# Kernel tuning notes

Hardware: AMD Instinct MI355X
Metric: run time of the kernel (lower is better)

## Reference

```python
import jax, jax.numpy as jnp
import numpy as np

DIM = 1024
NUM_HEADS = 16
HEAD_DIM = DIM // NUM_HEADS
SCALE = 1.0 / float(np.sqrt(HEAD_DIM))


def setup_inputs() -> dict:
    key = jax.random.key(0)
    ks = jax.random.split(key, 8)
    b, n = 1, 4096
    x = jax.random.normal(ks[0], (b, n, DIM), dtype=jnp.float32)
    cos = jax.random.uniform(ks[1], (b, n, HEAD_DIM // 2), dtype=jnp.float32)
    sin = jax.random.uniform(ks[2], (b, n, HEAD_DIM // 2), dtype=jnp.float32)
    # qkv Linear(dim, 3*dim) and proj Linear(dim, dim); store weights as [in, out]
    w_qkv = jax.random.normal(ks[3], (DIM, 3 * DIM), dtype=jnp.float32) * (1.0 / np.sqrt(DIM))
    b_qkv = jax.random.normal(ks[4], (3 * DIM,), dtype=jnp.float32) * 0.01
    w_proj = jax.random.normal(ks[5], (DIM, DIM), dtype=jnp.float32) * (1.0 / np.sqrt(DIM))
    b_proj = jax.random.normal(ks[6], (DIM,), dtype=jnp.float32) * 0.01
    return {"x": x, "cos": cos, "sin": sin, "w_qkv": w_qkv, "b_qkv": b_qkv,
            "w_proj": w_proj, "b_proj": b_proj}


def _rotate_half(t):
    t1, t2 = jnp.split(t, 2, axis=-1)
    return jnp.concatenate([-t2, t1], axis=-1)


def reference(x, cos, sin, w_qkv, b_qkv, w_proj, b_proj):
    b, n, d = x.shape
    qkv = x @ w_qkv + b_qkv                      # [b, n, 3d]
    q, k, v = jnp.split(qkv, 3, axis=-1)
    # [b, n, h, hd] layout (avoids explicit transposes; einsum handles head axis)
    q = q.reshape(b, n, NUM_HEADS, HEAD_DIM)
    k = k.reshape(b, n, NUM_HEADS, HEAD_DIM)
    v = v.reshape(b, n, NUM_HEADS, HEAD_DIM)
    # RoPE: cos/sin [b, n, hd/2] -> [b, n, 1, hd], broadcast over heads
    cos_f = jnp.concatenate([cos, cos], axis=-1)[:, :, None, :]
    sin_f = jnp.concatenate([sin, sin], axis=-1)[:, :, None, :]
    q = q * cos_f + _rotate_half(q) * sin_f
    k = k * cos_f + _rotate_half(k) * sin_f
    # SDPA (non-causal, no dropout in eval)
    scores = jnp.einsum("bqhd,bkhd->bhqk", q, k) * SCALE
    attn = jax.nn.softmax(scores, axis=-1)
    out = jnp.einsum("bhqk,bkhd->bqhd", attn, v).reshape(b, n, d)
    return out @ w_proj + b_proj
```

## Files before the change

### kernel.cpp

```cpp
#include <hip/hip_runtime.h>
#include <hip/hip_bf16.h>
#include <cstdint>


#define TOK 4096
#define DIM_ 1024
#define NHEAD 16
#define HDIM 64
#define N3 3072
#define SCALE_LOG2E 0.18033688011112042f

typedef __bf16 bf16_t;
typedef bf16_t bf16x8 __attribute__((ext_vector_type(8)));
typedef float floatx4 __attribute__((ext_vector_type(4)));

__device__ __forceinline__ void async_ld16(const bf16_t* g, bf16_t* l) {
  __builtin_amdgcn_global_load_lds(
      (const __attribute__((address_space(1))) void*)(g),
      (__attribute__((address_space(3))) void*)(l), 16, 0, 0);
}

__device__ __forceinline__ uint32_t pk2(float lo, float hi) {
  union { bf16_t b[2]; uint32_t u; } p;
  p.b[0] = (bf16_t)lo; p.b[1] = (bf16_t)hi;
  return p.u;
}

__global__ __launch_bounds__(256) void k_prep(
    const float* __restrict__ x, const float* __restrict__ w_qkv,
    const float* __restrict__ w_proj, bf16_t* __restrict__ xb,
    bf16_t* __restrict__ wqkvT, bf16_t* __restrict__ wprojT) {
  __shared__ float tile[32][33];
  const int b = blockIdx.x;
  if (b < 4096) {
    int i = b * 256 + threadIdx.x;
    float4 v = ((const float4*)x)[i];
    union { bf16_t bb[4]; uint64_t u; } p;
    p.bb[0] = (bf16_t)v.x; p.bb[1] = (bf16_t)v.y;
    p.bb[2] = (bf16_t)v.z; p.bb[3] = (bf16_t)v.w;
    ((uint64_t*)xb)[i] = p.u;
    return;
  }
  const float* in; bf16_t* out; int R, C, c0, r0;
  if (b < 7168) {
    int bb = b - 4096; in = w_qkv; out = wqkvT; R = 1024; C = 3072;
    c0 = (bb % 96) * 32; r0 = (bb / 96) * 32;
  } else {
    int bb = b - 7168; in = w_proj; out = wprojT; R = 1024; C = 1024;
    c0 = (bb % 32) * 32; r0 = (bb / 32) * 32;
  }
  int tx = threadIdx.x & 31, ty = threadIdx.x >> 5;
#pragma unroll
  for (int i = 0; i < 4; i++) {
    int r = ty + i * 8;
    tile[r][tx] = in[(size_t)(r0 + r) * C + c0 + tx];
  }
  __syncthreads();
#pragma unroll
  for (int i = 0; i < 4; i++) {
    int c = ty + i * 8;
    out[(size_t)(c0 + c) * R + r0 + tx] = (bf16_t)tile[tx][c];
  }
}

__global__ __launch_bounds__(256) void k_qkv(
    const bf16_t* __restrict__ A,
    const bf16_t* __restrict__ Bt,
    const float* __restrict__ bias,
    const float* __restrict__ cs,
    const float* __restrict__ sn,
    bf16_t* __restrict__ qb, bf16_t* __restrict__ kb, bf16_t* __restrict__ vT) {
  constexpr int K = 1024, BK = 32;
  __shared__ bf16_t As[128 * BK] __attribute__((aligned(16)));
  __shared__ bf16_t Bs[128 * BK] __attribute__((aligned(16)));
  const int t = threadIdx.x;
  const int lane = t & 63, w = t >> 6;
  const int lrow = lane & 15, quad = lane >> 4;
  const int m0 = blockIdx.y * 128, n0 = blockIdx.x * 128;
  const int wm = (w >> 1) * 64, wn = (w & 1) * 64;

  const floatx4 ZV = {0.f, 0.f, 0.f, 0.f};
  floatx4 acc[4][4];
#pragma unroll
  for (int i = 0; i < 4; i++)
#pragma unroll
    for (int j = 0; j < 4; j++) acc[i][j] = ZV;

  for (int kt = 0; kt < K; kt += BK) {
#pragma unroll
    for (int r = 0; r < 2; r++) {
      int idx = r * 256 + t;
      int lbase = (r * 256 + w * 64) * 8;
      async_ld16(&A[(size_t)(m0 + (idx >> 2)) * K + kt + (idx & 3) * 8], &As[lbase]);
      async_ld16(&Bt[(size_t)(n0 + (idx >> 2)) * K + kt + (idx & 3) * 8], &Bs[lbase]);
    }
    __syncthreads();
    bf16x8 af[4], bf[4];
#pragma unroll
    for (int i = 0; i < 4; i++)
      af[i] = *(const bf16x8*)&As[(wm + i * 16 + lrow) * BK + quad * 8];
#pragma unroll
    for (int i = 0; i < 4; i++)
      bf[i] = *(const bf16x8*)&Bs[(wn + i * 16 + lrow) * BK + quad * 8];
#pragma unroll
    for (int mi = 0; mi < 4; mi++)
#pragma unroll
      for (int ni = 0; ni < 4; ni++)
        acc[mi][ni] = __builtin_amdgcn_mfma_f32_16x16x32_bf16(af[mi], bf[ni], acc[mi][ni], 0, 0, 0);
    __syncthreads();
  }

  const int c0 = n0 + wn;
  const int seg = c0 >> 10;
  const int h = (c0 & 1023) >> 6;
  float bv[4];
#pragma unroll
  for (int ni = 0; ni < 4; ni++) bv[ni] = bias[c0 + ni * 16 + lrow];

  if (seg < 2) {
    bf16_t* base = ((seg == 0) ? qb : kb) + (size_t)h * TOK * HDIM;
    const float qs = (seg == 0) ? SCALE_LOG2E : 1.0f;
#pragma unroll
    for (int mi = 0; mi < 4; mi++) {
#pragma unroll
      for (int reg = 0; reg < 4; reg++) {
        const int r = m0 + wm + mi * 16 + quad * 4 + reg;
        const float c_lo = cs[r * 32 + lrow];
        const float c_hi = cs[r * 32 + 16 + lrow];
        const float s_lo = sn[r * 32 + lrow];
        const float s_hi = sn[r * 32 + 16 + lrow];
        const float v0 = acc[mi][0][reg] + bv[0];
        const float v1 = acc[mi][1][reg] + bv[1];
        const float v2 = acc[mi][2][reg] + bv[2];
        const float v3 = acc[mi][3][reg] + bv[3];
        const float o0 = (v0 * c_lo - v2 * s_lo) * qs;
        const float o1 = (v1 * c_hi - v3 * s_hi) * qs;
        const float o2 = (v2 * c_lo + v0 * s_lo) * qs;
        const float o3 = (v3 * c_hi + v1 * s_hi) * qs;
        bf16_t* rp = base + (size_t)r * HDIM + lrow;
        rp[0]  = (bf16_t)o0;
        rp[16] = (bf16_t)o1;
        rp[32] = (bf16_t)o2;
        rp[48] = (bf16_t)o3;
      }
    }
  } else {
    bf16_t* base = vT + (size_t)h * HDIM * TOK;
#pragma unroll
    for (int mi = 0; mi < 4; mi++) {
      const int rbase = m0 + wm + mi * 16 + quad * 4;
#pragma unroll
      for (int ni = 0; ni < 4; ni++) {
        union { bf16_t b[4]; uint64_t u; } p;
#pragma unroll
        for (int reg = 0; reg < 4; reg++) p.b[reg] = (bf16_t)(acc[mi][ni][reg] + bv[ni]);
        *(uint64_t*)&base[(size_t)(ni * 16 + lrow) * TOK + rbase] = p.u;
      }
    }
  }
}

__global__ __launch_bounds__(256, 2) void k_attn(
    const bf16_t* __restrict__ qb, const bf16_t* __restrict__ kb,
    const bf16_t* __restrict__ vT, bf16_t* __restrict__ ao) {
  __shared__ bf16_t Ks[2][64 * 64] __attribute__((aligned(16)));
  __shared__ bf16_t Vs[3][64 * 64] __attribute__((aligned(16)));
  __shared__ float Lmrg[128];
  const int t = threadIdx.x, lane = t & 63, w = t >> 6;
  const int lrow = lane & 15, quad = lane >> 4;
  const int qg = w & 1, kh = w >> 1;
  const int h = blockIdx.x & 15;
  const int q0 = (blockIdx.x >> 4) * 128;
  const bf16_t* qh = qb + (size_t)h * TOK * HDIM;
  const bf16_t* khp = kb + (size_t)h * TOK * HDIM;
  const bf16_t* vhp = vT + (size_t)h * HDIM * TOK;

  const int ksrc = (t >> 3) * HDIM + (((t & 7) ^ ((t >> 3) & 7)) * 8);
  const int vsrc = (t >> 3) * TOK + (((t & 7) ^ ((t >> 3) & 7)) * 8);

  bf16x8 qf[4][2];
#pragma unroll
  for (int ni = 0; ni < 4; ni++)
#pragma unroll
    for (int ks = 0; ks < 2; ks++)
      qf[ni][ks] = *(const bf16x8*)&qh[(size_t)(q0 + qg * 64 + ni * 16 + lrow) * HDIM + ks * 32 + quad * 8];

  const floatx4 ZV = {0.f, 0.f, 0.f, 0.f};
  floatx4 o[4][4];
  floatx4 lacc[4] = {ZV, ZV, ZV, ZV};
#pragma unroll
  for (int d = 0; d < 4; d++)
#pragma unroll
    for (int ni = 0; ni < 4; ni++) o[d][ni] = ZV;

#pragma unroll
  for (int r = 0; r < 2; r++) {
    async_ld16(&khp[(size_t)(r * 32) * HDIM + ksrc], &Ks[0][r * 2048 + t * 8]);
    async_ld16(&vhp[(size_t)(r * 32) * TOK + vsrc], &Vs[0][r * 2048 + t * 8]);
  }

  bf16x8 pf[4];
  bf16x8 vf[4];

  for (int it = 0; it < TOK / 64; ++it) {
    const int b = it & 1;
    __syncthreads();
    if (it + 1 < TOK / 64) {
      const int j1 = (it + 1) * 64;
      const int vs1 = (it + 1) % 3;
#pragma unroll
      for (int r = 0; r < 2; r++) {
        async_ld16(&khp[((size_t)j1 + r * 32) * HDIM + ksrc], &Ks[b ^ 1][r * 2048 + t * 8]);
        async_ld16(&vhp[(size_t)(r * 32) * TOK + j1 + vsrc], &Vs[vs1][r * 2048 + t * 8]);
      }
    }

    if (it > 0) {
#pragma unroll
      for (int dt = 0; dt < 4; dt++)
#pragma unroll
        for (int ni = 0; ni < 4; ni++)
          o[dt][ni] = __builtin_amdgcn_mfma_f32_16x16x32_bf16(vf[dt], pf[ni], o[dt][ni], 0, 0, 0);
    }

    floatx4 s[2][4];
#pragma unroll
    for (int mi = 0; mi < 2; mi++)
#pragma unroll
      for (int ni = 0; ni < 4; ni++) s[mi][ni] = ZV;
#pragma unroll
    for (int ks = 0; ks < 2; ks++)
#pragma unroll
      for (int mi = 0; mi < 2; mi++) {
        bf16x8 kf = *(const bf16x8*)&Ks[b][(kh * 32 + mi * 16 + lrow) * 64 + (((ks * 4 + quad) ^ (lrow & 7)) * 8)];
#pragma unroll
        for (int ni = 0; ni < 4; ni++)
          s[mi][ni] = __builtin_amdgcn_mfma_f32_16x16x32_bf16(kf, qf[ni][ks], s[mi][ni], 0, 0, 0);
      }

#pragma unroll
    for (int dt = 0; dt < 4; dt++)
      vf[dt] = *(const bf16x8*)&Vs[it % 3][(dt * 16 + lrow) * 64 + (((kh * 4 + quad) ^ (lrow & 7)) * 8)];

#pragma unroll
    for (int mi = 0; mi < 2; mi++)
#pragma unroll
      for (int ni = 0; ni < 4; ni++) {
#pragma unroll
        for (int reg = 0; reg < 4; reg++)
          s[mi][ni][reg] = __builtin_amdgcn_exp2f(s[mi][ni][reg]);
        lacc[ni] += s[mi][ni];
      }

#pragma unroll
    for (int ni = 0; ni < 4; ni++) {
      uint32_t A0 = pk2(s[0][ni][0], s[0][ni][1]);
      uint32_t A1 = pk2(s[0][ni][2], s[0][ni][3]);
      uint32_t B0 = pk2(s[1][ni][0], s[1][ni][1]);
      uint32_t B1 = pk2(s[1][ni][2], s[1][ni][3]);
      auto u0 = __builtin_amdgcn_permlane32_swap(A0, B0, false, false);
      auto u1 = __builtin_amdgcn_permlane32_swap(A1, B1, false, false);
      auto c0 = __builtin_amdgcn_permlane16_swap(u0[0], u0[1], false, false);
      auto c1 = __builtin_amdgcn_permlane16_swap(u1[0], u1[1], false, false);
      union { uint32_t d[4]; bf16x8 v; } pp;
      pp.d[0] = c0[0]; pp.d[1] = c1[0]; pp.d[2] = c0[1]; pp.d[3] = c1[1];
      pf[ni] = pp.v;
    }
  }

#pragma unroll
  for (int dt = 0; dt < 4; dt++)
#pragma unroll
    for (int ni = 0; ni < 4; ni++)
      o[dt][ni] = __builtin_amdgcn_mfma_f32_16x16x32_bf16(vf[dt], pf[ni], o[dt][ni], 0, 0, 0);

  __syncthreads();
  float* Mrg = (qg == 0) ? (float*)&Ks[0][0] : (float*)&Vs[0][0];
  float lq[4];
#pragma unroll
  for (int ni = 0; ni < 4; ni++) {
    float l = lacc[ni][0] + lacc[ni][1] + lacc[ni][2] + lacc[ni][3];
    l += __shfl_xor(l, 16, 64);
    l += __shfl_xor(l, 32, 64);
    lq[ni] = l;
  }
  if (kh == 1) {
#pragma unroll
    for (int ni = 0; ni < 4; ni++) {
#pragma unroll
      for (int dt = 0; dt < 4; dt++)
        *(floatx4*)&Mrg[(ni * 16 + lrow) * 64 + dt * 16 + quad * 4] = o[dt][ni];
      if (quad == 0) Lmrg[qg * 64 + ni * 16 + lrow] = lq[ni];
    }
  }
  __syncthreads();
  if (kh == 0) {
#pragma unroll
    for (int ni = 0; ni < 4; ni++) {
      const float l = lq[ni] + Lmrg[qg * 64 + ni * 16 + lrow];
      const float inv = 1.0f / l;
      const int qrow = q0 + qg * 64 + ni * 16 + lrow;
#pragma unroll
      for (int dt = 0; dt < 4; dt++) {
        floatx4 ov = *(const floatx4*)&Mrg[(ni * 16 + lrow) * 64 + dt * 16 + quad * 4];
        union { bf16_t b4[4]; uint64_t u; } p;
#pragma unroll
        for (int reg = 0; reg < 4; reg++) p.b4[reg] = (bf16_t)((o[dt][ni][reg] + ov[reg]) * inv);
        *(uint64_t*)&ao[(size_t)qrow * DIM_ + h * HDIM + dt * 16 + quad * 4] = p.u;
      }
    }
  }
}

__global__ __launch_bounds__(256) void k_proj(
    const bf16_t* __restrict__ A,
    const bf16_t* __restrict__ Bt,
    const float* __restrict__ bias, float* __restrict__ out) {
  constexpr int K = 1024, BK = 32;
  __shared__ bf16_t As[64 * BK] __attribute__((aligned(16)));
  __shared__ bf16_t Bs[128 * BK] __attribute__((aligned(16)));
  const int t = threadIdx.x;
  const int lane = t & 63, w = t >> 6;
  const int lrow = lane & 15, quad = lane >> 4;
  const int m0 = blockIdx.y * 64, n0 = blockIdx.x * 128;
  const int wm = (w >> 1) * 32, wn = (w & 1) * 64;

  const floatx4 ZV = {0.f, 0.f, 0.f, 0.f};
  floatx4 acc[2][4];
#pragma unroll
  for (int i = 0; i < 2; i++)
#pragma unroll
    for (int j = 0; j < 4; j++) acc[i][j] = ZV;

  for (int kt = 0; kt < K; kt += BK) {
    async_ld16(&A[(size_t)(m0 + (t >> 2)) * K + kt + (t & 3) * 8], &As[w * 512]);
#pragma unroll
    for (int r = 0; r < 2; r++) {
      int idx = r * 256 + t;
      async_ld16(&Bt[(size_t)(n0 + (idx >> 2)) * K + kt + (idx & 3) * 8],
                 &Bs[(r * 256 + w * 64) * 8]);
    }
    __syncthreads();
    bf16x8 af[2], bf[4];
#pragma unroll
    for (int i = 0; i < 2; i++)
      af[i] = *(const bf16x8*)&As[(wm + i * 16 + lrow) * BK + quad * 8];
#pragma unroll
    for (int i = 0; i < 4; i++)
      bf[i] = *(const bf16x8*)&Bs[(wn + i * 16 + lrow) * BK + quad * 8];
#pragma unroll
    for (int mi = 0; mi < 2; mi++)
#pragma unroll
      for (int ni = 0; ni < 4; ni++)
        acc[mi][ni] = __builtin_amdgcn_mfma_f32_16x16x32_bf16(af[mi], bf[ni], acc[mi][ni], 0, 0, 0);
    __syncthreads();
  }

  const int c0 = n0 + wn;
#pragma unroll
  for (int ni = 0; ni < 4; ni++) {
    float bv = bias[c0 + ni * 16 + lrow];
#pragma unroll
    for (int mi = 0; mi < 2; mi++)
#pragma unroll
      for (int reg = 0; reg < 4; reg++) {
        int r = m0 + wm + mi * 16 + quad * 4 + reg;
        out[(size_t)r * DIM_ + c0 + ni * 16 + lrow] = acc[mi][ni][reg] + bv;
      }
  }
}

extern "C" void kernel_launch(void* const* d_in, const int* in_sizes, int n_in,
                              void* d_out, int out_size, void* d_ws, size_t ws_size,
                              hipStream_t stream) {
  const float* x      = (const float*)d_in[0];
  const float* cs     = (const float*)d_in[1];
  const float* sn     = (const float*)d_in[2];
  const float* w_qkv  = (const float*)d_in[3];
  const float* b_qkv  = (const float*)d_in[4];
  const float* w_proj = (const float*)d_in[5];
  const float* b_proj = (const float*)d_in[6];
  float* out = (float*)d_out;

  char* ws = (char*)d_ws;
  bf16_t* xb     = (bf16_t*)(ws);
  bf16_t* wqkvT  = (bf16_t*)(ws + 8388608);
  bf16_t* wprojT = (bf16_t*)(ws + 14680064);
  bf16_t* qb     = (bf16_t*)(ws + 16777216);
  bf16_t* kb     = (bf16_t*)(ws + 25165824);
  bf16_t* vT     = (bf16_t*)(ws + 33554432);
  bf16_t* ao     = xb;

  k_prep<<<dim3(8192), dim3(256), 0, stream>>>(x, w_qkv, w_proj, xb, wqkvT, wprojT);
  k_qkv<<<dim3(24, 32), dim3(256), 0, stream>>>(xb, wqkvT, b_qkv, cs, sn, qb, kb, vT);
  k_attn<<<dim3(512), dim3(256), 0, stream>>>(qb, kb, vT, ao);
  k_proj<<<dim3(8, 64), dim3(256), 0, stream>>>(ao, wprojT, b_proj, out);
}
```

Before: 226.9 us.

## Enlarge attention blocks to 512 threads with 256 queries sharing K/V tiles

The attention kernel now runs 8 waves per block covering 256 query rows, so each K/V tile loaded into LDS serves twice as many queries. The V buffer drops from triple to double buffering, and the V fragment read moves ahead of the QK MFMAs. MFMA sections are wrapped in s_setprio raises. The final merge of the two key-half partial sums is done in two passes because the reused LDS only holds half the waves' outputs at once. The risks are fewer blocks (256) to spread across the CUs, more barriers, and less slack in prefetching V.

Result: no change. 227.6 us (+0.3%).

```diff
diff --git a/kernel.cpp b/kernel.cpp
--- a/kernel.cpp
+++ b/kernel.cpp
@@ -160,17 +160,17 @@
   }
 }
 
-__global__ __launch_bounds__(256, 2) void k_attn(
+__global__ __launch_bounds__(512, 2) void k_attn(
     const bf16_t* __restrict__ qb, const bf16_t* __restrict__ kb,
     const bf16_t* __restrict__ vT, bf16_t* __restrict__ ao) {
   __shared__ bf16_t Ks[2][64 * 64] __attribute__((aligned(16)));
-  __shared__ bf16_t Vs[3][64 * 64] __attribute__((aligned(16)));
-  __shared__ float Lmrg[128];
+  __shared__ bf16_t Vs[2][64 * 64] __attribute__((aligned(16)));
+  __shared__ float Lmrg[256];
   const int t = threadIdx.x, lane = t & 63, w = t >> 6;
   const int lrow = lane & 15, quad = lane >> 4;
-  const int qg = w & 1, kh = w >> 1;
+  const int qg = w >> 1, kh = w & 1;
   const int h = blockIdx.x & 15;
-  const int q0 = (blockIdx.x >> 4) * 128;
+  const int q0 = (blockIdx.x >> 4) * 256;
   const bf16_t* qh = qb + (size_t)h * TOK * HDIM;
   const bf16_t* khp = kb + (size_t)h * TOK * HDIM;
   const bf16_t* vhp = vT + (size_t)h * HDIM * TOK;
@@ -193,11 +193,8 @@
 #pragma unroll
     for (int ni = 0; ni < 4; ni++) o[d][ni] = ZV;
 
-#pragma unroll
-  for (int r = 0; r < 2; r++) {
-    async_ld16(&khp[(size_t)(r * 32) * HDIM + ksrc], &Ks[0][r * 2048 + t * 8]);
-    async_ld16(&vhp[(size_t)(r * 32) * TOK + vsrc], &Vs[0][r * 2048 + t * 8]);
-  }
+  async_ld16(&khp[ksrc], &Ks[0][t * 8]);
+  async_ld16(&vhp[vsrc], &Vs[0][t * 8]);
 
   bf16x8 pf[4];
   bf16x8 vf[4];
@@ -206,28 +203,31 @@
     const int b = it & 1;
     __syncthreads();
     if (it + 1 < TOK / 64) {
-      const int j1 = (it + 1) * 64;
-      const int vs1 = (it + 1) % 3;
-#pragma unroll
-      for (int r = 0; r < 2; r++) {
-        async_ld16(&khp[((size_t)j1 + r * 32) * HDIM + ksrc], &Ks[b ^ 1][r * 2048 + t * 8]);
-        async_ld16(&vhp[(size_t)(r * 32) * TOK + j1 + vsrc], &Vs[vs1][r * 2048 + t * 8]);
-      }
+      const size_t j1 = (size_t)(it + 1) * 64;
+      async_ld16(&khp[j1 * HDIM + ksrc], &Ks[b ^ 1][t * 8]);
+      async_ld16(&vhp[j1 + vsrc], &Vs[b ^ 1][t * 8]);
     }
 
     if (it > 0) {
+      __builtin_amdgcn_s_setprio(1);
 #pragma unroll
       for (int dt = 0; dt < 4; dt++)
 #pragma unroll
         for (int ni = 0; ni < 4; ni++)
           o[dt][ni] = __builtin_amdgcn_mfma_f32_16x16x32_bf16(vf[dt], pf[ni], o[dt][ni], 0, 0, 0);
-    }
+      __builtin_amdgcn_s_setprio(0);
+    }
+
+#pragma unroll
+    for (int dt = 0; dt < 4; dt++)
+      vf[dt] = *(const bf16x8*)&Vs[b][(dt * 16 + lrow) * 64 + (((kh * 4 + quad) ^ (lrow & 7)) * 8)];
 
     floatx4 s[2][4];
 #pragma unroll
     for (int mi = 0; mi < 2; mi++)
 #pragma unroll
       for (int ni = 0; ni < 4; ni++) s[mi][ni] = ZV;
+    __builtin_amdgcn_s_setprio(1);
 #pragma unroll
     for (int ks = 0; ks < 2; ks++)
 #pragma unroll
@@ -237,10 +237,7 @@
         for (int ni = 0; ni < 4; ni++)
           s[mi][ni] = __builtin_amdgcn_mfma_f32_16x16x32_bf16(kf, qf[ni][ks], s[mi][ni], 0, 0, 0);
       }
-
-#pragma unroll
-    for (int dt = 0; dt < 4; dt++)
-      vf[dt] = *(const bf16x8*)&Vs[it % 3][(dt * 16 + lrow) * 64 + (((kh * 4 + quad) ^ (lrow & 7)) * 8)];
+    __builtin_amdgcn_s_setprio(0);
 
 #pragma unroll
     for (int mi = 0; mi < 2; mi++)
@@ -275,7 +272,6 @@
       o[dt][ni] = __builtin_amdgcn_mfma_f32_16x16x32_bf16(vf[dt], pf[ni], o[dt][ni], 0, 0, 0);
 
   __syncthreads();
-  float* Mrg = (qg == 0) ? (float*)&Ks[0][0] : (float*)&Vs[0][0];
   float lq[4];
 #pragma unroll
   for (int ni = 0; ni < 4; ni++) {
@@ -284,31 +280,38 @@
     l += __shfl_xor(l, 32, 64);
     lq[ni] = l;
   }
-  if (kh == 1) {
-#pragma unroll
-    for (int ni = 0; ni < 4; ni++) {
-#pragma unroll
-      for (int dt = 0; dt < 4; dt++)
-        *(floatx4*)&Mrg[(ni * 16 + lrow) * 64 + dt * 16 + quad * 4] = o[dt][ni];
-      if (quad == 0) Lmrg[qg * 64 + ni * 16 + lrow] = lq[ni];
-    }
-  }
-  __syncthreads();
-  if (kh == 0) {
-#pragma unroll
-    for (int ni = 0; ni < 4; ni++) {
-      const float l = lq[ni] + Lmrg[qg * 64 + ni * 16 + lrow];
-      const float inv = 1.0f / l;
-      const int qrow = q0 + qg * 64 + ni * 16 + lrow;
-#pragma unroll
-      for (int dt = 0; dt < 4; dt++) {
-        floatx4 ov = *(const floatx4*)&Mrg[(ni * 16 + lrow) * 64 + dt * 16 + quad * 4];
-        union { bf16_t b4[4]; uint64_t u; } p;
-#pragma unroll
-        for (int reg = 0; reg < 4; reg++) p.b4[reg] = (bf16_t)((o[dt][ni][reg] + ov[reg]) * inv);
-        *(uint64_t*)&ao[(size_t)qrow * DIM_ + h * HDIM + dt * 16 + quad * 4] = p.u;
-      }
-    }
+  if (kh == 1 && quad == 0) {
+#pragma unroll
+    for (int ni = 0; ni < 4; ni++) Lmrg[qg * 64 + ni * 16 + lrow] = lq[ni];
+  }
+  float* Mrg = (qg & 1) ? (float*)&Vs[0][0] : (float*)&Ks[0][0];
+#pragma unroll
+  for (int p = 0; p < 2; ++p) {
+    if ((qg >> 1) == p && kh == 1) {
+#pragma unroll
+      for (int ni = 0; ni < 4; ni++)
+#pragma unroll
+        for (int dt = 0; dt < 4; dt++)
+          *(floatx4*)&Mrg[(ni * 16 + lrow) * 64 + dt * 16 + quad * 4] = o[dt][ni];
+    }
+    __syncthreads();
+    if ((qg >> 1) == p && kh == 0) {
+#pragma unroll
+      for (int ni = 0; ni < 4; ni++) {
+        const float l = lq[ni] + Lmrg[qg * 64 + ni * 16 + lrow];
+        const float inv = 1.0f / l;
+        const int qrow = q0 + qg * 64 + ni * 16 + lrow;
+#pragma unroll
+        for (int dt = 0; dt < 4; dt++) {
+          floatx4 ov = *(const floatx4*)&Mrg[(ni * 16 + lrow) * 64 + dt * 16 + quad * 4];
+          union { bf16_t b4[4]; uint64_t u; } pq;
+#pragma unroll
+          for (int reg = 0; reg < 4; reg++) pq.b4[reg] = (bf16_t)((o[dt][ni][reg] + ov[reg]) * inv);
+          *(uint64_t*)&ao[(size_t)qrow * DIM_ + h * HDIM + dt * 16 + quad * 4] = pq.u;
+        }
+      }
+    }
+    __syncthreads();
   }
 }
 
@@ -393,6 +396,6 @@
 
   k_prep<<<dim3(8192), dim3(256), 0, stream>>>(x, w_qkv, w_proj, xb, wqkvT, wprojT);
   k_qkv<<<dim3(24, 32), dim3(256), 0, stream>>>(xb, wqkvT, b_qkv, cs, sn, qb, kb, vT);
-  k_attn<<<dim3(512), dim3(256), 0, stream>>>(qb, kb, vT, ao);
+  k_attn<<<dim3(256), dim3(512), 0, stream>>>(qb, kb, vT, ao);
   k_proj<<<dim3(8, 64), dim3(256), 0, stream>>>(ao, wprojT, b_proj, out);
 }
```
